# Kernel tuning notes

Hardware: AMD Instinct MI355X
Metric: run time of the kernel (lower is better)

Reference implementation:

```python
import jax, jax.numpy as jnp
import numpy as np

N_NONZERO = 32      # n_nonzero_coefs
TAU = 0.01
LAMBDA_INIT = -5.0  # reg_coeff = softplus(lambda)


def setup_inputs() -> dict:
    key = jax.random.key(0)
    k1, k2 = jax.random.split(key)
    X = jax.random.normal(k1, (64, 1024, 1024), dtype=jnp.float32)
    y = jax.random.normal(k2, (64, 1024, 1), dtype=jnp.float32)
    return {"X": X, "y": y}


def _omp_fit_forward(X, y):
    # Faithful translation of fit() (omp with hard straight-through top-1)
    # followed by forward() reconstruction D @ coef.
    reg = jax.nn.softplus(jnp.asarray(LAMBDA_INIT, jnp.float32)).astype(X.dtype)
    B, L, A = X.shape
    ones = jnp.ones((B, L, 1), X.dtype)
    Dfull = jnp.concatenate([X, ones], axis=-1)   # [B, L, A+1] (bias column)
    D = Dfull[0]                                   # shared dictionary [L, A+1]
    n_atoms = A + 1
    y2 = y[:, :, 0]                                # [B, L]
    y_det = jax.lax.stop_gradient(y2)
    residuals = y_det
    # Cache selected_D columns incrementally: each column j is dict @ ret_j,
    # identical math to the original's full recompute every iteration.
    selD = jnp.zeros((B, L, N_NONZERO), X.dtype)
    idx_all = []
    nzW = None
    for i in range(N_NONZERO):
        proj = residuals @ D                                      # [B, A+1]
        soft = jax.nn.softmax(jnp.abs(proj) / TAU, axis=-1)
        idx = jnp.argmax(jnp.abs(proj), axis=-1)                  # detached indices
        onehot = jax.nn.one_hot(jnp.argmax(soft, axis=-1), n_atoms, dtype=X.dtype)
        ret = onehot - jax.lax.stop_gradient(soft) + soft         # straight-through
        new_col = ret @ D.T                                       # [B, L]
        selD = selD.at[:, :, i].set(new_col)
        Di = selD[:, :, :i + 1]                                   # [B, L, i+1]
        DTy = jnp.einsum('blk,bl->bk', Di, y2)[..., None]         # [B, i+1, 1]
        DTD = jnp.einsum('blk,blj->bkj', Di, Di) + reg * jnp.eye(i + 1, dtype=X.dtype)
        nzW = jnp.linalg.solve(DTD, DTy)                          # [B, i+1, 1]
        residuals = y_det - jnp.einsum('blk,bk->bl', Di, nzW[..., 0])
        idx_all.append(idx)
    indices = jnp.stack(idx_all, axis=1)                          # [B, K] int
    W = jnp.zeros((B, n_atoms), X.dtype).at[jnp.arange(B)[:, None], indices].set(nzW[..., 0])
    # forward(): bmm(dict_with_bias, coef)
    recon = jnp.einsum('bla,ba->bl', Dfull, W)[..., None]         # [B, L, 1]
    return recon


def reference(X, y):
    return _omp_fit_forward(X, y)
```

## Files before the change

kernel.cpp:

```cpp
#include <hip/hip_runtime.h>
#include <math.h>

#define NATOMS   1025
#define GSTRIDE  1040
#define GELEMS   (1025*GSTRIDE)
#define NNZ      32
#define NBATCH   64
#define REGL     0.0067153485f

#define DPPF(x, ctrl) __int_as_float(__builtin_amdgcn_update_dpp(0, __float_as_int(x), (ctrl), 0xF, 0xF, false))

__device__ __forceinline__ float wave_max64(float x) {
    x = fmaxf(x, DPPF(x, 0x111));
    x = fmaxf(x, DPPF(x, 0x112));
    x = fmaxf(x, DPPF(x, 0x114));
    x = fmaxf(x, DPPF(x, 0x118));
    x = fmaxf(x, DPPF(x, 0x142));
    x = fmaxf(x, DPPF(x, 0x143));
    return __int_as_float(__builtin_amdgcn_readlane(__float_as_int(x), 63));
}
__device__ __forceinline__ float wave_sum64(float x) {
    x += DPPF(x, 0x111);
    x += DPPF(x, 0x112);
    x += DPPF(x, 0x114);
    x += DPPF(x, 0x118);
    x += DPPF(x, 0x142);
    x += DPPF(x, 0x143);
    return __int_as_float(__builtin_amdgcn_readlane(__float_as_int(x), 63));
}
__device__ __forceinline__ float readlane_f(float x, int l) {
    return __int_as_float(__builtin_amdgcn_readlane(__float_as_int(x), l));
}

__global__ __launch_bounds__(256)
void gramprojy_kernel(const float* __restrict__ X0, const float* __restrict__ y,
                      float* __restrict__ Gout, float* __restrict__ PY,
                      int kLen, int nsplit) {
    __shared__ float lds[8192];
    const int tid = threadIdx.x;

    if ((int)blockIdx.z < nsplit) {
        const int bx = blockIdx.x, by = blockIdx.y, bz = blockIdx.z;
        if (by < bx) return;
        float* As = lds;
        float* Bs = lds + 4096;
        const int a0 = bx * 128, b0 = by * 128;
        float* __restrict__ Gp = Gout + (size_t)bz * GELEMS;
        const int tx = tid & 15;
        const int ty = tid >> 4;
        const int lr = tid >> 5;
        const int lc = (tid & 31) * 4;
        const bool aIn = (a0 + 128) <= 1024;
        const bool bIn = (b0 + 128) <= 1024;

        float acc[8][8];
#pragma unroll
        for (int m = 0; m < 8; ++m)
#pragma unroll
            for (int n = 0; n < 8; ++n) acc[m][n] = 0.0f;

        const int kBase = bz * kLen;
        for (int kc = 0; kc < kLen; kc += 32) {
#pragma unroll
            for (int rr = 0; rr < 4; ++rr) {
                const int r = lr + rr * 8;
                const int l = kBase + kc + r;
                if (aIn) {
                    *(float4*)&As[r * 128 + lc] = *(const float4*)&X0[(size_t)l * 1024 + a0 + lc];
                } else {
#pragma unroll
                    for (int k = 0; k < 4; ++k) {
                        const int col = a0 + lc + k;
                        As[r * 128 + lc + k] = (col < 1024) ? X0[(size_t)l * 1024 + col]
                                                            : (col == 1024 ? 1.0f : 0.0f);
                    }
                }
                if (bIn) {
                    *(float4*)&Bs[r * 128 + lc] = *(const float4*)&X0[(size_t)l * 1024 + b0 + lc];
                } else {
#pragma unroll
                    for (int k = 0; k < 4; ++k) {
                        const int col = b0 + lc + k;
                        Bs[r * 128 + lc + k] = (col < 1024) ? X0[(size_t)l * 1024 + col]
                                                            : (col == 1024 ? 1.0f : 0.0f);
                    }
                }
            }
            __syncthreads();
#pragma unroll 8
            for (int l = 0; l < 32; ++l) {
                float4 a01 = *(const float4*)&As[l * 128 + ty * 8];
                float4 a23 = *(const float4*)&As[l * 128 + ty * 8 + 4];
                float4 bA  = *(const float4*)&Bs[l * 128 + tx * 4];
                float4 bB  = *(const float4*)&Bs[l * 128 + 64 + tx * 4];
                float am[8] = {a01.x, a01.y, a01.z, a01.w, a23.x, a23.y, a23.z, a23.w};
                float bn[8] = {bA.x, bA.y, bA.z, bA.w, bB.x, bB.y, bB.z, bB.w};
#pragma unroll
                for (int m = 0; m < 8; ++m)
#pragma unroll
                    for (int n = 0; n < 8; ++n)
                        acc[m][n] += am[m] * bn[n];
            }
            __syncthreads();
        }

#pragma unroll
        for (int m = 0; m < 8; ++m) {
            const int a = a0 + ty * 8 + m;
            if (a >= NATOMS) continue;
            const int bAc = b0 + tx * 4;
            const int bBc = b0 + 64 + tx * 4;
            if (bAc < GSTRIDE) {
                *(float4*)&Gp[(size_t)a * GSTRIDE + bAc] =
                    make_float4(acc[m][0], acc[m][1], acc[m][2], acc[m][3]);
            }
            if (bBc < GSTRIDE) {
                *(float4*)&Gp[(size_t)a * GSTRIDE + bBc] =
                    make_float4(acc[m][4], acc[m][5], acc[m][6], acc[m][7]);
            }
        }
        if (bx != by) {
#pragma unroll
            for (int n = 0; n < 8; ++n) {
                const int colg = b0 + ((n < 4) ? (tx * 4 + n) : (64 + tx * 4 + (n - 4)));
                if (colg >= NATOMS) continue;
                const int a = a0 + ty * 8;
                *(float4*)&Gp[(size_t)colg * GSTRIDE + a] =
                    make_float4(acc[0][n], acc[1][n], acc[2][n], acc[3][n]);
                *(float4*)&Gp[(size_t)colg * GSTRIDE + a + 4] =
                    make_float4(acc[4][n], acc[5][n], acc[6][n], acc[7][n]);
            }
        }
    } else {
        const int pw = blockIdx.y * 9 + blockIdx.x;
        if (pw >= 68) return;
        const int a0 = (pw % 17) * 64;
        const int b0 = (pw / 17) * 16;
        float* Ds = lds;
        float* Ys = lds + 2048;
        const int tx = tid & 15;
        const int ty = tid >> 4;
        const bool aIn = (a0 + 64) <= 1024;

        float acc[4] = {0.0f, 0.0f, 0.0f, 0.0f};

        for (int kc = 0; kc < 1024; kc += 32) {
            {
                const int r  = tid >> 4;
                const int c4 = (tid & 15) * 4;
#pragma unroll
                for (int rr = 0; rr < 2; ++rr) {
                    const int row = r + rr * 16;
                    const int l = kc + row;
                    if (aIn) {
                        *(float4*)&Ds[row * 64 + c4] = *(const float4*)&X0[(size_t)l * 1024 + a0 + c4];
                    } else {
#pragma unroll
                        for (int k = 0; k < 4; ++k) {
                            const int col = a0 + c4 + k;
                            Ds[row * 64 + c4 + k] = (col < 1024) ? X0[(size_t)l * 1024 + col]
                                                                 : (col == 1024 ? 1.0f : 0.0f);
                        }
                    }
                }
            }
            for (int e = tid; e < 512; e += 256) {
                const int l = e & 31, bb = e >> 5;
                Ys[l * 17 + bb] = y[(size_t)(b0 + bb) * 1024 + kc + l];
            }
            __syncthreads();
#pragma unroll 8
            for (int l = 0; l < 32; ++l) {
                const float yv = Ys[l * 17 + ty];
                float4 dv = *(const float4*)&Ds[l * 64 + tx * 4];
                acc[0] += yv * dv.x; acc[1] += yv * dv.y;
                acc[2] += yv * dv.z; acc[3] += yv * dv.w;
            }
            __syncthreads();
        }
        const int a = a0 + tx * 4;
        if (a < GSTRIDE) {
            *(float4*)&PY[(size_t)(b0 + ty) * GSTRIDE + a] =
                make_float4(acc[0], acc[1], acc[2], acc[3]);
        }
    }
}

template <int NS>
__global__ __launch_bounds__(512)
void omp_kernel(const float* __restrict__ Gp, const float* __restrict__ PY,
                int* __restrict__ idxOut, float* __restrict__ wOut) {
    __shared__ float rowsLds[NNZ][GSTRIDE];
    __shared__ float pyLds[1040];
    __shared__ float diagLds[1040];
    __shared__ float redV[2][8];
    __shared__ int   redI[2][8];

    const int b = blockIdx.x, tid = threadIdx.x;
    const int lane = tid & 63, wid = tid >> 6;

    float ainv[32];
#pragma unroll
    for (int m = 0; m < 32; ++m) ainv[m] = 0.0f;
    float wvr = 0.0f, rhsr = 0.0f;
    int   myIdx = 0;

    {
        float4 z4 = make_float4(0.f, 0.f, 0.f, 0.f);
        float4* rz = (float4*)rowsLds;
        for (int u = tid; u < NNZ * GSTRIDE / 4; u += 512) rz[u] = z4;
        const float* pyg = PY + (size_t)b * GSTRIDE;
        for (int u = tid; u < 1040; u += 512) pyLds[u] = pyg[u];
        float d0 = 0.f, d1 = 0.f, d2 = 0.f;
#pragma unroll
        for (int z = 0; z < NS; ++z) {
            const float* gz = Gp + (size_t)z * GELEMS;
            d0 += gz[(size_t)tid * (GSTRIDE + 1)];
            d1 += gz[(size_t)(tid + 512) * (GSTRIDE + 1)];
            if (tid == 511) d2 += gz[(size_t)1024 * (GSTRIDE + 1)];
        }
        diagLds[tid] = d0;
        diagLds[tid + 512] = d1;
        if (tid == 511) diagLds[1024] = d2;
    }
    __syncthreads();

    float p0 = pyLds[tid], p1 = pyLds[tid + 512];
    float p2 = (tid == 511) ? pyLds[1024] : 0.0f;

    {
        float best = fabsf(p0); int bidx = tid;
        { float v = fabsf(p1); if (v > best) { best = v; bidx = tid + 512; } }
        if (tid == 511) { float v = fabsf(p2); if (v > best) { best = v; bidx = 1024; } }
        const float wmax = wave_max64(best);
        const unsigned long long mask = __ballot(best == wmax);
        const int fl = __ffsll((unsigned long long)mask) - 1;
        const int widx = __builtin_amdgcn_readlane(bidx, fl);
        if (lane == 0) { redV[0][wid] = wmax; redI[0][wid] = widx; }
    }
    __syncthreads();

    for (int i = 0; i < NNZ; ++i) {
        const int par = i & 1;

        float bv_ = redV[par][0]; int sel = redI[par][0];
#pragma unroll
        for (int q = 1; q < 8; ++q) {
            if (redV[par][q] > bv_ || (redV[par][q] == bv_ && redI[par][q] < sel)) {
                bv_ = redV[par][q]; sel = redI[par][q];
            }
        }
        const float pysel = pyLds[sel];

        float rA0 = 0.f, rA1 = 0.f, rA2 = 0.f, rA3 = 0.f;
        float rB0 = 0.f, rB1 = 0.f, rB2 = 0.f, rB3 = 0.f;
        float rA4 = 0.f, rA5 = 0.f, rA6 = 0.f, rA7 = 0.f;
        float rB4 = 0.f, rB5 = 0.f, rB6 = 0.f, rB7 = 0.f;
        float rC = 0.f;
        if (i < NNZ - 1) {
            const size_t rowoff = (size_t)sel * GSTRIDE;
            const float* g0 = Gp + rowoff;
            rA0 = g0[tid];            rB0 = g0[tid + 512];
            if (NS > 1) { const float* g = g0 + (size_t)1 * GELEMS; rA1 = g[tid]; rB1 = g[tid + 512]; }
            if (NS > 2) { const float* g = g0 + (size_t)2 * GELEMS; rA2 = g[tid]; rB2 = g[tid + 512]; }
            if (NS > 3) { const float* g = g0 + (size_t)3 * GELEMS; rA3 = g[tid]; rB3 = g[tid + 512]; }
            if (NS > 4) { const float* g = g0 + (size_t)4 * GELEMS; rA4 = g[tid]; rB4 = g[tid + 512]; }
            if (NS > 5) { const float* g = g0 + (size_t)5 * GELEMS; rA5 = g[tid]; rB5 = g[tid + 512]; }
            if (NS > 6) { const float* g = g0 + (size_t)6 * GELEMS; rA6 = g[tid]; rB6 = g[tid + 512]; }
            if (NS > 7) { const float* g = g0 + (size_t)7 * GELEMS; rA7 = g[tid]; rB7 = g[tid + 512]; }
            if (tid == 511) {
#pragma unroll
                for (int z = 0; z < NS; ++z) rC += Gp[(size_t)z * GELEMS + rowoff + 1024];
            }
        }

        const float bvl = (lane < 32) ? rowsLds[lane][sel] : 0.0f;
        float u0 = 0.f, u1 = 0.f, u2 = 0.f, u3 = 0.f;
#pragma unroll
        for (int m = 0; m < 32; m += 4) {
            u0 = fmaf(ainv[m + 0], rowsLds[m + 0][sel], u0);
            u1 = fmaf(ainv[m + 1], rowsLds[m + 1][sel], u1);
            u2 = fmaf(ainv[m + 2], rowsLds[m + 2][sel], u2);
            u3 = fmaf(ainv[m + 3], rowsLds[m + 3][sel], u3);
        }
        const float uacc = (u0 + u1) + (u2 + u3);
        const float t = wave_sum64(bvl * uacc);
        const float s = wave_sum64(rhsr * uacc);
        const float dinv = 1.0f / (diagLds[sel] + REGL - t);
        const float beta = dinv * (pysel - s);
        const float uvb = (lane == i) ? -1.0f : uacc;
#pragma unroll
        for (int m = 0; m < 32; ++m)
            ainv[m] = fmaf(uvb * dinv, readlane_f(uvb, m), ainv[m]);
        wvr = (lane == i) ? beta : fmaf(-uacc, beta, wvr);
        rhsr = (lane == i) ? pysel : rhsr;
        if (tid == i) myIdx = sel;

        if (i == NNZ - 1) break;

        float z0 = 0.f, z1 = 0.f, z2 = 0.f;
        for (int jb = 0; jb < NNZ; jb += 8) {
            if (jb >= i) break;
#pragma unroll
            for (int jj = 0; jj < 8; ++jj) {
                const int j = jb + jj;
                const float uj = readlane_f(uvb, j);
                z0 = fmaf(uj, rowsLds[j][tid],       z0);
                z1 = fmaf(uj, rowsLds[j][tid + 512], z1);
                if (tid == 511) z2 = fmaf(uj, rowsLds[j][1024], z2);
            }
        }
        const float r0 = ((rA0 + rA1) + (rA2 + rA3)) + ((rA4 + rA5) + (rA6 + rA7));
        const float r1 = ((rB0 + rB1) + (rB2 + rB3)) + ((rB4 + rB5) + (rB6 + rB7));
        p0 = fmaf(beta, z0, p0); p0 = fmaf(-beta, r0, p0);
        p1 = fmaf(beta, z1, p1); p1 = fmaf(-beta, r1, p1);
        if (tid == 511) { p2 = fmaf(beta, z2, p2); p2 = fmaf(-beta, rC, p2); }

        rowsLds[i][tid]       = r0;
        rowsLds[i][tid + 512] = r1;
        if (tid == 511) rowsLds[i][1024] = rC;

        {
            float best = fabsf(p0); int bidx = tid;
            { float v = fabsf(p1); if (v > best) { best = v; bidx = tid + 512; } }
            if (tid == 511) { float v = fabsf(p2); if (v > best) { best = v; bidx = 1024; } }
            const float wmax = wave_max64(best);
            const unsigned long long mask = __ballot(best == wmax);
            const int fl = __ffsll((unsigned long long)mask) - 1;
            const int widx = __builtin_amdgcn_readlane(bidx, fl);
            if (lane == 0) { redV[par ^ 1][wid] = wmax; redI[par ^ 1][wid] = widx; }
        }
        __syncthreads();
    }

    if (tid < NNZ) {
        idxOut[b * NNZ + tid] = myIdx;
        wOut[b * NNZ + tid] = wvr;
    }
}

__global__ __launch_bounds__(256)
void recon_kernel(const float* __restrict__ X, const int* __restrict__ idxIn,
                  const float* __restrict__ wIn, float* __restrict__ out) {
    __shared__ float Wd[1025];
    __shared__ float wval[NNZ];
    __shared__ int   widx[NNZ];
    __shared__ float biasS;
    const int b = blockIdx.x >> 2, chunk = blockIdx.x & 3;
    const int tid = threadIdx.x;
    for (int u = tid; u < 1025; u += 256) Wd[u] = 0.0f;
    __syncthreads();
    if (tid == 0) {
#pragma unroll
        for (int i = 0; i < NNZ; ++i) Wd[idxIn[b * NNZ + i]] = wIn[b * NNZ + i];
        float bias = 0.0f;
#pragma unroll
        for (int i = 0; i < NNZ; ++i) {
            const int gi = idxIn[b * NNZ + i];
            const float v = Wd[gi];
            Wd[gi] = 0.0f;
            const bool isOnes = (gi == 1024);
            if (isOnes) bias += v;
            widx[i] = isOnes ? 0 : gi;
            wval[i] = isOnes ? 0.0f : v;
        }
        biasS = bias;
    }
    __syncthreads();
    const int l = chunk * 256 + tid;
    const float* __restrict__ xr = X + (size_t)b * 1024 * 1024 + (size_t)l * 1024;
    float a0 = biasS, a1 = 0.f, a2 = 0.f, a3 = 0.f;
#pragma unroll
    for (int i = 0; i < NNZ; i += 4) {
        a0 = fmaf(xr[widx[i + 0]], wval[i + 0], a0);
        a1 = fmaf(xr[widx[i + 1]], wval[i + 1], a1);
        a2 = fmaf(xr[widx[i + 2]], wval[i + 2], a2);
        a3 = fmaf(xr[widx[i + 3]], wval[i + 3], a3);
    }
    out[(size_t)b * 1024 + l] = (a0 + a1) + (a2 + a3);
}

extern "C" void kernel_launch(void* const* d_in, const int* in_sizes, int n_in,
                              void* d_out, int out_size, void* d_ws, size_t ws_size,
                              hipStream_t stream) {
    const float* X = (const float*)d_in[0];
    const float* y = (const float*)d_in[1];
    float* out = (float*)d_out;
    float* ws = (float*)d_ws;

    const size_t fixed = (size_t)64 * GSTRIDE + NBATCH * NNZ * 2 + 64;
    const size_t need8 = ((size_t)GELEMS * 8 + fixed) * sizeof(float);
    const size_t need4 = ((size_t)GELEMS * 4 + fixed) * sizeof(float);
    const int nsplit = (ws_size >= need8) ? 8 : ((ws_size >= need4) ? 4 : 1);
    const int kLen = 1024 / nsplit;

    float* Gp = ws;
    float* PY = ws + (size_t)GELEMS * nsplit;
    float* wOut = PY + (size_t)64 * GSTRIDE;
    int* idxOut = (int*)(wOut + NBATCH * NNZ);

    gramprojy_kernel<<<dim3(9, 9, nsplit + 1), 256, 0, stream>>>(X, y, Gp, PY, kLen, nsplit);
    if (nsplit == 8)      omp_kernel<8><<<NBATCH, 512, 0, stream>>>(Gp, PY, idxOut, wOut);
    else if (nsplit == 4) omp_kernel<4><<<NBATCH, 512, 0, stream>>>(Gp, PY, idxOut, wOut);
    else                  omp_kernel<1><<<NBATCH, 512, 0, stream>>>(Gp, PY, idxOut, wOut);
    recon_kernel<<<NBATCH * 4, 256, 0, stream>>>(X, idxOut, wOut, out);
}
```

Before: 221.2 us.

## Keep selected Gram rows in registers and fully unroll OMP iterations

Each thread now holds the 32 selected Gram-row entries for its two columns in register arrays instead of a 32x1040 LDS table, and the iteration loop is fully unrolled by macro so those arrays can be indexed statically. The selected column's entries are broadcast through a small shared vector, which adds an extra barrier per iteration. The maximum Gram split drops from 8 to 4, so the partial-Gram reduction per row load does less work but the Gram build runs with fewer splits. Register pressure rises sharply (64 extra floats per thread at 512 threads), which risks spills.

```diff
diff --git a/kernel.cpp b/kernel.cpp
--- a/kernel.cpp
+++ b/kernel.cpp
@@ -190,27 +190,28 @@
 __global__ __launch_bounds__(512)
 void omp_kernel(const float* __restrict__ Gp, const float* __restrict__ PY,
                 int* __restrict__ idxOut, float* __restrict__ wOut) {
-    __shared__ float rowsLds[NNZ][GSTRIDE];
     __shared__ float pyLds[1040];
     __shared__ float diagLds[1040];
+    __shared__ float bvec[32];
+    __shared__ float row1024[NNZ];
     __shared__ float redV[2][8];
     __shared__ int   redI[2][8];
 
     const int b = blockIdx.x, tid = threadIdx.x;
     const int lane = tid & 63, wid = tid >> 6;
 
+    float rr0[NNZ], rr1[NNZ];
     float ainv[32];
 #pragma unroll
-    for (int m = 0; m < 32; ++m) ainv[m] = 0.0f;
-    float wvr = 0.0f, rhsr = 0.0f;
+    for (int m = 0; m < 32; ++m) { ainv[m] = 0.f; rr0[m] = 0.f; rr1[m] = 0.f; }
+    float wvr = 0.f, rhsr = 0.f;
     int   myIdx = 0;
 
     {
-        float4 z4 = make_float4(0.f, 0.f, 0.f, 0.f);
-        float4* rz = (float4*)rowsLds;
-        for (int u = tid; u < NNZ * GSTRIDE / 4; u += 512) rz[u] = z4;
         const float* pyg = PY + (size_t)b * GSTRIDE;
-        for (int u = tid; u < 1040; u += 512) pyLds[u] = pyg[u];
+        pyLds[tid] = pyg[tid];
+        pyLds[tid + 512] = pyg[tid + 512];
+        if (tid < 16) pyLds[1024 + tid] = pyg[1024 + tid];
         float d0 = 0.f, d1 = 0.f, d2 = 0.f;
 #pragma unroll
         for (int z = 0; z < NS; ++z) {
@@ -222,11 +223,12 @@
         diagLds[tid] = d0;
         diagLds[tid + 512] = d1;
         if (tid == 511) diagLds[1024] = d2;
+        if (tid < 32) { bvec[tid] = 0.f; row1024[tid] = 0.f; }
     }
     __syncthreads();
 
     float p0 = pyLds[tid], p1 = pyLds[tid + 512];
-    float p2 = (tid == 511) ? pyLds[1024] : 0.0f;
+    float p2 = (tid == 511) ? pyLds[1024] : 0.f;
 
     {
         float best = fabsf(p0); int bidx = tid;
@@ -240,98 +242,108 @@
     }
     __syncthreads();
 
-    for (int i = 0; i < NNZ; ++i) {
-        const int par = i & 1;
-
-        float bv_ = redV[par][0]; int sel = redI[par][0];
-#pragma unroll
-        for (int q = 1; q < 8; ++q) {
-            if (redV[par][q] > bv_ || (redV[par][q] == bv_ && redI[par][q] < sel)) {
-                bv_ = redV[par][q]; sel = redI[par][q];
-            }
-        }
-        const float pysel = pyLds[sel];
-
-        float rA0 = 0.f, rA1 = 0.f, rA2 = 0.f, rA3 = 0.f;
-        float rB0 = 0.f, rB1 = 0.f, rB2 = 0.f, rB3 = 0.f;
-        float rA4 = 0.f, rA5 = 0.f, rA6 = 0.f, rA7 = 0.f;
-        float rB4 = 0.f, rB5 = 0.f, rB6 = 0.f, rB7 = 0.f;
-        float rC = 0.f;
-        if (i < NNZ - 1) {
-            const size_t rowoff = (size_t)sel * GSTRIDE;
-            const float* g0 = Gp + rowoff;
-            rA0 = g0[tid];            rB0 = g0[tid + 512];
-            if (NS > 1) { const float* g = g0 + (size_t)1 * GELEMS; rA1 = g[tid]; rB1 = g[tid + 512]; }
-            if (NS > 2) { const float* g = g0 + (size_t)2 * GELEMS; rA2 = g[tid]; rB2 = g[tid + 512]; }
-            if (NS > 3) { const float* g = g0 + (size_t)3 * GELEMS; rA3 = g[tid]; rB3 = g[tid + 512]; }
-            if (NS > 4) { const float* g = g0 + (size_t)4 * GELEMS; rA4 = g[tid]; rB4 = g[tid + 512]; }
-            if (NS > 5) { const float* g = g0 + (size_t)5 * GELEMS; rA5 = g[tid]; rB5 = g[tid + 512]; }
-            if (NS > 6) { const float* g = g0 + (size_t)6 * GELEMS; rA6 = g[tid]; rB6 = g[tid + 512]; }
-            if (NS > 7) { const float* g = g0 + (size_t)7 * GELEMS; rA7 = g[tid]; rB7 = g[tid + 512]; }
-            if (tid == 511) {
-#pragma unroll
-                for (int z = 0; z < NS; ++z) rC += Gp[(size_t)z * GELEMS + rowoff + 1024];
-            }
-        }
-
-        const float bvl = (lane < 32) ? rowsLds[lane][sel] : 0.0f;
-        float u0 = 0.f, u1 = 0.f, u2 = 0.f, u3 = 0.f;
-#pragma unroll
-        for (int m = 0; m < 32; m += 4) {
-            u0 = fmaf(ainv[m + 0], rowsLds[m + 0][sel], u0);
-            u1 = fmaf(ainv[m + 1], rowsLds[m + 1][sel], u1);
-            u2 = fmaf(ainv[m + 2], rowsLds[m + 2][sel], u2);
-            u3 = fmaf(ainv[m + 3], rowsLds[m + 3][sel], u3);
-        }
-        const float uacc = (u0 + u1) + (u2 + u3);
-        const float t = wave_sum64(bvl * uacc);
-        const float s = wave_sum64(rhsr * uacc);
-        const float dinv = 1.0f / (diagLds[sel] + REGL - t);
-        const float beta = dinv * (pysel - s);
-        const float uvb = (lane == i) ? -1.0f : uacc;
-#pragma unroll
-        for (int m = 0; m < 32; ++m)
-            ainv[m] = fmaf(uvb * dinv, readlane_f(uvb, m), ainv[m]);
-        wvr = (lane == i) ? beta : fmaf(-uacc, beta, wvr);
-        rhsr = (lane == i) ? pysel : rhsr;
-        if (tid == i) myIdx = sel;
-
-        if (i == NNZ - 1) break;
-
-        float z0 = 0.f, z1 = 0.f, z2 = 0.f;
-        for (int jb = 0; jb < NNZ; jb += 8) {
-            if (jb >= i) break;
-#pragma unroll
-            for (int jj = 0; jj < 8; ++jj) {
-                const int j = jb + jj;
-                const float uj = readlane_f(uvb, j);
-                z0 = fmaf(uj, rowsLds[j][tid],       z0);
-                z1 = fmaf(uj, rowsLds[j][tid + 512], z1);
-                if (tid == 511) z2 = fmaf(uj, rowsLds[j][1024], z2);
-            }
-        }
-        const float r0 = ((rA0 + rA1) + (rA2 + rA3)) + ((rA4 + rA5) + (rA6 + rA7));
-        const float r1 = ((rB0 + rB1) + (rB2 + rB3)) + ((rB4 + rB5) + (rB6 + rB7));
-        p0 = fmaf(beta, z0, p0); p0 = fmaf(-beta, r0, p0);
-        p1 = fmaf(beta, z1, p1); p1 = fmaf(-beta, r1, p1);
-        if (tid == 511) { p2 = fmaf(beta, z2, p2); p2 = fmaf(-beta, rC, p2); }
-
-        rowsLds[i][tid]       = r0;
-        rowsLds[i][tid + 512] = r1;
-        if (tid == 511) rowsLds[i][1024] = rC;
-
-        {
-            float best = fabsf(p0); int bidx = tid;
-            { float v = fabsf(p1); if (v > best) { best = v; bidx = tid + 512; } }
-            if (tid == 511) { float v = fabsf(p2); if (v > best) { best = v; bidx = 1024; } }
-            const float wmax = wave_max64(best);
-            const unsigned long long mask = __ballot(best == wmax);
-            const int fl = __ffsll((unsigned long long)mask) - 1;
-            const int widx = __builtin_amdgcn_readlane(bidx, fl);
-            if (lane == 0) { redV[par ^ 1][wid] = wmax; redI[par ^ 1][wid] = widx; }
-        }
-        __syncthreads();
-    }
+#define OMP_ITER(I)                                                            \
+    {                                                                          \
+        const int par = (I) & 1;                                               \
+        float bv_ = redV[par][0]; int sel = redI[par][0];                      \
+        _Pragma("unroll")                                                      \
+        for (int q = 1; q < 8; ++q) {                                          \
+            if (redV[par][q] > bv_ ||                                          \
+                (redV[par][q] == bv_ && redI[par][q] < sel)) {                 \
+                bv_ = redV[par][q]; sel = redI[par][q];                        \
+            }                                                                  \
+        }                                                                      \
+        const float pysel = pyLds[sel];                                        \
+        float rA0=0.f,rA1=0.f,rA2=0.f,rA3=0.f;                                 \
+        float rB0=0.f,rB1=0.f,rB2=0.f,rB3=0.f,rC=0.f;                          \
+        if ((I) < NNZ - 1) {                                                   \
+            const size_t ro = (size_t)sel * GSTRIDE;                           \
+            { const float* g = Gp + ro; rA0 = g[tid]; rB0 = g[tid + 512]; }    \
+            if (NS > 1) { const float* g = Gp + ro + (size_t)1 * GELEMS;       \
+                          rA1 = g[tid]; rB1 = g[tid + 512]; }                  \
+            if (NS > 2) { const float* g = Gp + ro + (size_t)2 * GELEMS;       \
+                          rA2 = g[tid]; rB2 = g[tid + 512]; }                  \
+            if (NS > 3) { const float* g = Gp + ro + (size_t)3 * GELEMS;       \
+                          rA3 = g[tid]; rB3 = g[tid + 512]; }                  \
+            if (tid == 511) {                                                  \
+                _Pragma("unroll")                                              \
+                for (int z = 0; z < NS; ++z)                                   \
+                    rC += Gp[(size_t)z * GELEMS + ro + 1024];                  \
+            }                                                                  \
+        }                                                                      \
+        if (sel == 1024) {                                                     \
+            if (tid < 32) bvec[tid] = row1024[tid];                            \
+        } else if (tid == (sel & 511)) {                                       \
+            if (sel >> 9) {                                                    \
+                _Pragma("unroll")                                              \
+                for (int m = 0; m < 32; ++m) bvec[m] = rr1[m];                 \
+            } else {                                                           \
+                _Pragma("unroll")                                              \
+                for (int m = 0; m < 32; ++m) bvec[m] = rr0[m];                 \
+            }                                                                  \
+        }                                                                      \
+        __syncthreads();                               \
+        const float bvl = (lane < 32) ? bvec[lane] : 0.f;                      \
+        float u0 = 0.f, u1 = 0.f;                                              \
+        _Pragma("unroll")                                                      \
+        for (int m = 0; m < 32; m += 2) {                                      \
+            u0 = fmaf(ainv[m],     bvec[m],     u0);                           \
+            u1 = fmaf(ainv[m + 1], bvec[m + 1], u1);                           \
+        }                                                                      \
+        const float uacc = u0 + u1;                                            \
+        const float t = wave_sum64(bvl * uacc);                                \
+        const float s = wave_sum64(rhsr * uacc);                               \
+        const float dinv = 1.0f / (diagLds[sel] + REGL - t);                   \
+        const float beta = dinv * (pysel - s);                                 \
+        const float uvb = (lane == (I)) ? -1.0f : uacc;                        \
+        _Pragma("unroll")                                                      \
+        for (int m = 0; m < 32; ++m)                                           \
+            ainv[m] = fmaf(uvb * dinv, readlane_f(uvb, m), ainv[m]);           \
+        wvr  = (lane == (I)) ? beta  : fmaf(-uacc, beta, wvr);                 \
+        rhsr = (lane == (I)) ? pysel : rhsr;                                   \
+        if (tid == (I)) myIdx = sel;                                           \
+        if ((I) < NNZ - 1) {                                                   \
+            float z0 = 0.f, z1 = 0.f, z2 = 0.f;                                \
+            _Pragma("unroll")                                                  \
+            for (int j = 0; j < NNZ - 1; ++j) {                                \
+                if (j < (I)) {                                                 \
+                    const float uj = readlane_f(uvb, j);                       \
+                    z0 = fmaf(uj, rr0[j], z0);                                 \
+                    z1 = fmaf(uj, rr1[j], z1);                                 \
+                    if (tid == 511) z2 = fmaf(uj, row1024[j], z2);             \
+                }                                                              \
+            }                                                                  \
+            const float r0 = (rA0 + rA1) + (rA2 + rA3);                        \
+            const float r1 = (rB0 + rB1) + (rB2 + rB3);                        \
+            p0 = fmaf(beta, z0, p0); p0 = fmaf(-beta, r0, p0);                 \
+            p1 = fmaf(beta, z1, p1); p1 = fmaf(-beta, r1, p1);                 \
+            if (tid == 511) { p2 = fmaf(beta, z2, p2);                         \
+                              p2 = fmaf(-beta, rC, p2); }                      \
+            rr0[(I)] = r0; rr1[(I)] = r1;                                      \
+            if (tid == 511) row1024[(I)] = rC;                                 \
+            float best = fabsf(p0); int bidx = tid;                            \
+            { float v = fabsf(p1); if (v > best) { best = v; bidx = tid + 512; } } \
+            if (tid == 511) { float v = fabsf(p2);                             \
+                              if (v > best) { best = v; bidx = 1024; } }       \
+            const float wmax = wave_max64(best);                               \
+            const unsigned long long mask = __ballot(best == wmax);            \
+            const int fl = __ffsll((unsigned long long)mask) - 1;              \
+            const int widx = __builtin_amdgcn_readlane(bidx, fl);              \
+            if (lane == 0) { redV[par ^ 1][wid] = wmax;                        \
+                             redI[par ^ 1][wid] = widx; }                      \
+            __syncthreads();                    \
+        }                                                                      \
+    }
+
+    OMP_ITER(0)  OMP_ITER(1)  OMP_ITER(2)  OMP_ITER(3)
+    OMP_ITER(4)  OMP_ITER(5)  OMP_ITER(6)  OMP_ITER(7)
+    OMP_ITER(8)  OMP_ITER(9)  OMP_ITER(10) OMP_ITER(11)
+    OMP_ITER(12) OMP_ITER(13) OMP_ITER(14) OMP_ITER(15)
+    OMP_ITER(16) OMP_ITER(17) OMP_ITER(18) OMP_ITER(19)
+    OMP_ITER(20) OMP_ITER(21) OMP_ITER(22) OMP_ITER(23)
+    OMP_ITER(24) OMP_ITER(25) OMP_ITER(26) OMP_ITER(27)
+    OMP_ITER(28) OMP_ITER(29) OMP_ITER(30) OMP_ITER(31)
+#undef OMP_ITER
 
     if (tid < NNZ) {
         idxOut[b * NNZ + tid] = myIdx;
@@ -389,9 +401,8 @@
     float* ws = (float*)d_ws;
 
     const size_t fixed = (size_t)64 * GSTRIDE + NBATCH * NNZ * 2 + 64;
-    const size_t need8 = ((size_t)GELEMS * 8 + fixed) * sizeof(float);
     const size_t need4 = ((size_t)GELEMS * 4 + fixed) * sizeof(float);
-    const int nsplit = (ws_size >= need8) ? 8 : ((ws_size >= need4) ? 4 : 1);
+    const int nsplit = (ws_size >= need4) ? 4 : 1;
     const int kLen = 1024 / nsplit;
 
     float* Gp = ws;
@@ -400,8 +411,7 @@
     int* idxOut = (int*)(wOut + NBATCH * NNZ);
 
     gramprojy_kernel<<<dim3(9, 9, nsplit + 1), 256, 0, stream>>>(X, y, Gp, PY, kLen, nsplit);
-    if (nsplit == 8)      omp_kernel<8><<<NBATCH, 512, 0, stream>>>(Gp, PY, idxOut, wOut);
-    else if (nsplit == 4) omp_kernel<4><<<NBATCH, 512, 0, stream>>>(Gp, PY, idxOut, wOut);
-    else                  omp_kernel<1><<<NBATCH, 512, 0, stream>>>(Gp, PY, idxOut, wOut);
+    if (nsplit == 4) omp_kernel<4><<<NBATCH, 512, 0, stream>>>(Gp, PY, idxOut, wOut);
+    else             omp_kernel<1><<<NBATCH, 512, 0, stream>>>(Gp, PY, idxOut, wOut);
     recon_kernel<<<NBATCH * 4, 256, 0, stream>>>(X, idxOut, wOut, out);
 }
```

After: 179.8 us. 18.7% less time.

## Run OMP loop with one wavefront per batch and drop cross-wave reductions

Applied to the files above, without the earlier changes.

The OMP kernel now runs each batch on a single 64-lane wavefront instead of 512 threads. Each lane holds 16 projection values in registers and does the argmax fully inside the wave with DPP, so the LDS cross-wave reduction is gone. Rows of Ainv are gathered with readlane instead of LDS reads, and the Gram split count drops from 8 to at most 4, which lowers gram partial-sum traffic. The cost is far less parallelism per batch: 64 waves in total do the serial per-atom work, and the Gram row loads and the z accumulation are each spread over only 64 lanes.

```diff
diff --git a/kernel.cpp b/kernel.cpp
--- a/kernel.cpp
+++ b/kernel.cpp
@@ -4,21 +4,13 @@
 #define NATOMS   1025
 #define GSTRIDE  1040
 #define GELEMS   (1025*GSTRIDE)
+#define RSTRIDE  1026
 #define NNZ      32
 #define NBATCH   64
 #define REGL     0.0067153485f
 
 #define DPPF(x, ctrl) __int_as_float(__builtin_amdgcn_update_dpp(0, __float_as_int(x), (ctrl), 0xF, 0xF, false))
 
-__device__ __forceinline__ float wave_max64(float x) {
-    x = fmaxf(x, DPPF(x, 0x111));
-    x = fmaxf(x, DPPF(x, 0x112));
-    x = fmaxf(x, DPPF(x, 0x114));
-    x = fmaxf(x, DPPF(x, 0x118));
-    x = fmaxf(x, DPPF(x, 0x142));
-    x = fmaxf(x, DPPF(x, 0x143));
-    return __int_as_float(__builtin_amdgcn_readlane(__float_as_int(x), 63));
-}
 __device__ __forceinline__ float wave_sum64(float x) {
     x += DPPF(x, 0x111);
     x += DPPF(x, 0x112);
@@ -30,6 +22,17 @@
 }
 __device__ __forceinline__ float readlane_f(float x, int l) {
     return __int_as_float(__builtin_amdgcn_readlane(__float_as_int(x), l));
+}
+__device__ __forceinline__ void wave_argmax64(float& v, int& idx) {
+#define AM_STEP(ctrl) {                                                        \
+        float ov = DPPF(v, ctrl);                                              \
+        int   oi = __builtin_amdgcn_update_dpp(0, idx, (ctrl), 0xF, 0xF, false);\
+        if (ov > v || (ov == v && oi < idx)) { v = ov; idx = oi; } }
+    AM_STEP(0x111) AM_STEP(0x112) AM_STEP(0x114) AM_STEP(0x118)
+    AM_STEP(0x142) AM_STEP(0x143)
+#undef AM_STEP
+    v   = readlane_f(v, 63);
+    idx = __builtin_amdgcn_readlane(idx, 63);
 }
 
 __global__ __launch_bounds__(256)
@@ -187,103 +190,87 @@
 }
 
 template <int NS>
-__global__ __launch_bounds__(512)
+__global__ __launch_bounds__(64)
 void omp_kernel(const float* __restrict__ Gp, const float* __restrict__ PY,
                 int* __restrict__ idxOut, float* __restrict__ wOut) {
-    __shared__ float rowsLds[NNZ][GSTRIDE];
-    __shared__ float pyLds[1040];
-    __shared__ float diagLds[1040];
-    __shared__ float redV[2][8];
-    __shared__ int   redI[2][8];
-
-    const int b = blockIdx.x, tid = threadIdx.x;
-    const int lane = tid & 63, wid = tid >> 6;
+    __shared__ float rowsLds[NNZ][RSTRIDE];
+    __shared__ float pyLds[NATOMS];
+    __shared__ float diagLds[NATOMS];
+
+    const int b = blockIdx.x;
+    const int lane = threadIdx.x;
 
     float ainv[32];
 #pragma unroll
-    for (int m = 0; m < 32; ++m) ainv[m] = 0.0f;
-    float wvr = 0.0f, rhsr = 0.0f;
+    for (int m = 0; m < 32; ++m) ainv[m] = 0.f;
+    float wvr = 0.f, rhsr = 0.f;
     int   myIdx = 0;
 
     {
-        float4 z4 = make_float4(0.f, 0.f, 0.f, 0.f);
-        float4* rz = (float4*)rowsLds;
-        for (int u = tid; u < NNZ * GSTRIDE / 4; u += 512) rz[u] = z4;
+        float4* rz = (float4*)&rowsLds[0][0];
+        for (int u = lane; u < NNZ * RSTRIDE / 4; u += 64)
+            rz[u] = make_float4(0.f, 0.f, 0.f, 0.f);
         const float* pyg = PY + (size_t)b * GSTRIDE;
-        for (int u = tid; u < 1040; u += 512) pyLds[u] = pyg[u];
-        float d0 = 0.f, d1 = 0.f, d2 = 0.f;
-#pragma unroll
-        for (int z = 0; z < NS; ++z) {
-            const float* gz = Gp + (size_t)z * GELEMS;
-            d0 += gz[(size_t)tid * (GSTRIDE + 1)];
-            d1 += gz[(size_t)(tid + 512) * (GSTRIDE + 1)];
-            if (tid == 511) d2 += gz[(size_t)1024 * (GSTRIDE + 1)];
-        }
-        diagLds[tid] = d0;
-        diagLds[tid + 512] = d1;
-        if (tid == 511) diagLds[1024] = d2;
+        for (int u = lane; u < NATOMS; u += 64) {
+            pyLds[u] = pyg[u];
+            float d = 0.f;
+#pragma unroll
+            for (int z = 0; z < NS; ++z)
+                d += Gp[(size_t)z * GELEMS + (size_t)u * (GSTRIDE + 1)];
+            diagLds[u] = d;
+        }
     }
     __syncthreads();
 
-    float p0 = pyLds[tid], p1 = pyLds[tid + 512];
-    float p2 = (tid == 511) ? pyLds[1024] : 0.0f;
-
+    float2 pr[8];
+#pragma unroll
+    for (int k = 0; k < 8; ++k)
+        pr[k] = *(const float2*)&pyLds[2 * lane + 128 * k];
+    float p1024 = (lane == 0) ? pyLds[1024] : 0.f;
+
+    float bv; int sel;
     {
-        float best = fabsf(p0); int bidx = tid;
-        { float v = fabsf(p1); if (v > best) { best = v; bidx = tid + 512; } }
-        if (tid == 511) { float v = fabsf(p2); if (v > best) { best = v; bidx = 1024; } }
-        const float wmax = wave_max64(best);
-        const unsigned long long mask = __ballot(best == wmax);
-        const int fl = __ffsll((unsigned long long)mask) - 1;
-        const int widx = __builtin_amdgcn_readlane(bidx, fl);
-        if (lane == 0) { redV[0][wid] = wmax; redI[0][wid] = widx; }
-    }
-    __syncthreads();
+        bv = fabsf(pr[0].x); sel = 2 * lane;
+        { float v = fabsf(pr[0].y); if (v > bv) { bv = v; sel = 2 * lane + 1; } }
+#pragma unroll
+        for (int k = 1; k < 8; ++k) {
+            float vx = fabsf(pr[k].x);
+            if (vx > bv) { bv = vx; sel = 2 * lane + 128 * k; }
+            float vy = fabsf(pr[k].y);
+            if (vy > bv) { bv = vy; sel = 2 * lane + 128 * k + 1; }
+        }
+        if (lane == 0) { float v = fabsf(p1024); if (v > bv) { bv = v; sel = 1024; } }
+        wave_argmax64(bv, sel);
+    }
 
     for (int i = 0; i < NNZ; ++i) {
-        const int par = i & 1;
-
-        float bv_ = redV[par][0]; int sel = redI[par][0];
-#pragma unroll
-        for (int q = 1; q < 8; ++q) {
-            if (redV[par][q] > bv_ || (redV[par][q] == bv_ && redI[par][q] < sel)) {
-                bv_ = redV[par][q]; sel = redI[par][q];
-            }
-        }
         const float pysel = pyLds[sel];
 
-        float rA0 = 0.f, rA1 = 0.f, rA2 = 0.f, rA3 = 0.f;
-        float rB0 = 0.f, rB1 = 0.f, rB2 = 0.f, rB3 = 0.f;
-        float rA4 = 0.f, rA5 = 0.f, rA6 = 0.f, rA7 = 0.f;
-        float rB4 = 0.f, rB5 = 0.f, rB6 = 0.f, rB7 = 0.f;
-        float rC = 0.f;
+        float2 sv[8]; float s1024 = 0.f;
+#pragma unroll
+        for (int k = 0; k < 8; ++k) sv[k] = make_float2(0.f, 0.f);
         if (i < NNZ - 1) {
-            const size_t rowoff = (size_t)sel * GSTRIDE;
-            const float* g0 = Gp + rowoff;
-            rA0 = g0[tid];            rB0 = g0[tid + 512];
-            if (NS > 1) { const float* g = g0 + (size_t)1 * GELEMS; rA1 = g[tid]; rB1 = g[tid + 512]; }
-            if (NS > 2) { const float* g = g0 + (size_t)2 * GELEMS; rA2 = g[tid]; rB2 = g[tid + 512]; }
-            if (NS > 3) { const float* g = g0 + (size_t)3 * GELEMS; rA3 = g[tid]; rB3 = g[tid + 512]; }
-            if (NS > 4) { const float* g = g0 + (size_t)4 * GELEMS; rA4 = g[tid]; rB4 = g[tid + 512]; }
-            if (NS > 5) { const float* g = g0 + (size_t)5 * GELEMS; rA5 = g[tid]; rB5 = g[tid + 512]; }
-            if (NS > 6) { const float* g = g0 + (size_t)6 * GELEMS; rA6 = g[tid]; rB6 = g[tid + 512]; }
-            if (NS > 7) { const float* g = g0 + (size_t)7 * GELEMS; rA7 = g[tid]; rB7 = g[tid + 512]; }
-            if (tid == 511) {
-#pragma unroll
-                for (int z = 0; z < NS; ++z) rC += Gp[(size_t)z * GELEMS + rowoff + 1024];
-            }
-        }
-
-        const float bvl = (lane < 32) ? rowsLds[lane][sel] : 0.0f;
-        float u0 = 0.f, u1 = 0.f, u2 = 0.f, u3 = 0.f;
-#pragma unroll
-        for (int m = 0; m < 32; m += 4) {
-            u0 = fmaf(ainv[m + 0], rowsLds[m + 0][sel], u0);
-            u1 = fmaf(ainv[m + 1], rowsLds[m + 1][sel], u1);
-            u2 = fmaf(ainv[m + 2], rowsLds[m + 2][sel], u2);
-            u3 = fmaf(ainv[m + 3], rowsLds[m + 3][sel], u3);
-        }
-        const float uacc = (u0 + u1) + (u2 + u3);
+            const size_t ro = (size_t)sel * GSTRIDE;
+#pragma unroll
+            for (int z = 0; z < NS; ++z) {
+                const float* g = Gp + (size_t)z * GELEMS + ro;
+#pragma unroll
+                for (int k = 0; k < 8; ++k) {
+                    const float2 t2 = *(const float2*)(g + 2 * lane + 128 * k);
+                    sv[k].x += t2.x; sv[k].y += t2.y;
+                }
+                if (lane == 0) s1024 += g[1024];
+            }
+        }
+
+        const float bvl = (lane < 32) ? rowsLds[lane][sel] : 0.f;
+        float u0 = 0.f, u1 = 0.f;
+#pragma unroll
+        for (int m = 0; m < 32; m += 2) {
+            u0 = fmaf(ainv[m],     readlane_f(bvl, m),     u0);
+            u1 = fmaf(ainv[m + 1], readlane_f(bvl, m + 1), u1);
+        }
+        const float uacc = u0 + u1;
         const float t = wave_sum64(bvl * uacc);
         const float s = wave_sum64(rhsr * uacc);
         const float dinv = 1.0f / (diagLds[sel] + REGL - t);
@@ -292,50 +279,54 @@
 #pragma unroll
         for (int m = 0; m < 32; ++m)
             ainv[m] = fmaf(uvb * dinv, readlane_f(uvb, m), ainv[m]);
-        wvr = (lane == i) ? beta : fmaf(-uacc, beta, wvr);
+        wvr  = (lane == i) ? beta  : fmaf(-uacc, beta, wvr);
         rhsr = (lane == i) ? pysel : rhsr;
-        if (tid == i) myIdx = sel;
+        if (lane == i) myIdx = sel;
 
         if (i == NNZ - 1) break;
 
-        float z0 = 0.f, z1 = 0.f, z2 = 0.f;
-        for (int jb = 0; jb < NNZ; jb += 8) {
-            if (jb >= i) break;
-#pragma unroll
-            for (int jj = 0; jj < 8; ++jj) {
-                const int j = jb + jj;
-                const float uj = readlane_f(uvb, j);
-                z0 = fmaf(uj, rowsLds[j][tid],       z0);
-                z1 = fmaf(uj, rowsLds[j][tid + 512], z1);
-                if (tid == 511) z2 = fmaf(uj, rowsLds[j][1024], z2);
-            }
-        }
-        const float r0 = ((rA0 + rA1) + (rA2 + rA3)) + ((rA4 + rA5) + (rA6 + rA7));
-        const float r1 = ((rB0 + rB1) + (rB2 + rB3)) + ((rB4 + rB5) + (rB6 + rB7));
-        p0 = fmaf(beta, z0, p0); p0 = fmaf(-beta, r0, p0);
-        p1 = fmaf(beta, z1, p1); p1 = fmaf(-beta, r1, p1);
-        if (tid == 511) { p2 = fmaf(beta, z2, p2); p2 = fmaf(-beta, rC, p2); }
-
-        rowsLds[i][tid]       = r0;
-        rowsLds[i][tid + 512] = r1;
-        if (tid == 511) rowsLds[i][1024] = rC;
-
-        {
-            float best = fabsf(p0); int bidx = tid;
-            { float v = fabsf(p1); if (v > best) { best = v; bidx = tid + 512; } }
-            if (tid == 511) { float v = fabsf(p2); if (v > best) { best = v; bidx = 1024; } }
-            const float wmax = wave_max64(best);
-            const unsigned long long mask = __ballot(best == wmax);
-            const int fl = __ffsll((unsigned long long)mask) - 1;
-            const int widx = __builtin_amdgcn_readlane(bidx, fl);
-            if (lane == 0) { redV[par ^ 1][wid] = wmax; redI[par ^ 1][wid] = widx; }
-        }
+        float2 zz[8]; float z1024 = 0.f;
+#pragma unroll
+        for (int k = 0; k < 8; ++k) zz[k] = make_float2(0.f, 0.f);
+        for (int j = 0; j < i; ++j) {
+            const float uj = readlane_f(uvb, j);
+#pragma unroll
+            for (int k = 0; k < 8; ++k) {
+                const float2 g = *(const float2*)&rowsLds[j][2 * lane + 128 * k];
+                zz[k].x = fmaf(uj, g.x, zz[k].x);
+                zz[k].y = fmaf(uj, g.y, zz[k].y);
+            }
+            if (lane == 0) z1024 = fmaf(uj, rowsLds[j][1024], z1024);
+        }
+#pragma unroll
+        for (int k = 0; k < 8; ++k) {
+            pr[k].x = fmaf(beta, zz[k].x, pr[k].x); pr[k].x = fmaf(-beta, sv[k].x, pr[k].x);
+            pr[k].y = fmaf(beta, zz[k].y, pr[k].y); pr[k].y = fmaf(-beta, sv[k].y, pr[k].y);
+        }
+        if (lane == 0) { p1024 = fmaf(beta, z1024, p1024); p1024 = fmaf(-beta, s1024, p1024); }
+
+#pragma unroll
+        for (int k = 0; k < 8; ++k)
+            *(float2*)&rowsLds[i][2 * lane + 128 * k] = sv[k];
+        if (lane == 0) rowsLds[i][1024] = s1024;
         __syncthreads();
-    }
-
-    if (tid < NNZ) {
-        idxOut[b * NNZ + tid] = myIdx;
-        wOut[b * NNZ + tid] = wvr;
+
+        bv = fabsf(pr[0].x); sel = 2 * lane;
+        { float v = fabsf(pr[0].y); if (v > bv) { bv = v; sel = 2 * lane + 1; } }
+#pragma unroll
+        for (int k = 1; k < 8; ++k) {
+            float vx = fabsf(pr[k].x);
+            if (vx > bv) { bv = vx; sel = 2 * lane + 128 * k; }
+            float vy = fabsf(pr[k].y);
+            if (vy > bv) { bv = vy; sel = 2 * lane + 128 * k + 1; }
+        }
+        if (lane == 0) { float v = fabsf(p1024); if (v > bv) { bv = v; sel = 1024; } }
+        wave_argmax64(bv, sel);
+    }
+
+    if (lane < NNZ) {
+        idxOut[b * NNZ + lane] = myIdx;
+        wOut[b * NNZ + lane] = wvr;
     }
 }
 
@@ -389,9 +380,8 @@
     float* ws = (float*)d_ws;
 
     const size_t fixed = (size_t)64 * GSTRIDE + NBATCH * NNZ * 2 + 64;
-    const size_t need8 = ((size_t)GELEMS * 8 + fixed) * sizeof(float);
     const size_t need4 = ((size_t)GELEMS * 4 + fixed) * sizeof(float);
-    const int nsplit = (ws_size >= need8) ? 8 : ((ws_size >= need4) ? 4 : 1);
+    const int nsplit = (ws_size >= need4) ? 4 : 1;
     const int kLen = 1024 / nsplit;
 
     float* Gp = ws;
@@ -400,8 +390,7 @@
     int* idxOut = (int*)(wOut + NBATCH * NNZ);
 
     gramprojy_kernel<<<dim3(9, 9, nsplit + 1), 256, 0, stream>>>(X, y, Gp, PY, kLen, nsplit);
-    if (nsplit == 8)      omp_kernel<8><<<NBATCH, 512, 0, stream>>>(Gp, PY, idxOut, wOut);
-    else if (nsplit == 4) omp_kernel<4><<<NBATCH, 512, 0, stream>>>(Gp, PY, idxOut, wOut);
-    else                  omp_kernel<1><<<NBATCH, 512, 0, stream>>>(Gp, PY, idxOut, wOut);
+    if (nsplit == 4) omp_kernel<4><<<NBATCH, 64, 0, stream>>>(Gp, PY, idxOut, wOut);
+    else             omp_kernel<1><<<NBATCH, 64, 0, stream>>>(Gp, PY, idxOut, wOut);
     recon_kernel<<<NBATCH * 4, 256, 0, stream>>>(X, idxOut, wOut, out);
 }
```

Result: slower. 226.6 us (+2.5%).

## Transpose OMP column cache in LDS and cap Gram split at four

Applied to the files above, without the earlier changes.

Stores the cached Gram rows in LDS transposed (atom-major with stride 33), so gathering the selected atom's column and each thread's own history becomes a contiguous, bank-conflict-free read. The z accumulation loop now runs exactly i iterations instead of blocks of eight. The per-wave argmax becomes a fused value/index DPP reduction that drops the ballot step. The Gram split is capped at four partial slices, which halves the global row loads per OMP iteration but makes each partial GEMM in the first kernel longer.

```diff
diff --git a/kernel.cpp b/kernel.cpp
--- a/kernel.cpp
+++ b/kernel.cpp
@@ -4,21 +4,13 @@
 #define NATOMS   1025
 #define GSTRIDE  1040
 #define GELEMS   (1025*GSTRIDE)
+#define CSTRIDE  33
 #define NNZ      32
 #define NBATCH   64
 #define REGL     0.0067153485f
 
 #define DPPF(x, ctrl) __int_as_float(__builtin_amdgcn_update_dpp(0, __float_as_int(x), (ctrl), 0xF, 0xF, false))
 
-__device__ __forceinline__ float wave_max64(float x) {
-    x = fmaxf(x, DPPF(x, 0x111));
-    x = fmaxf(x, DPPF(x, 0x112));
-    x = fmaxf(x, DPPF(x, 0x114));
-    x = fmaxf(x, DPPF(x, 0x118));
-    x = fmaxf(x, DPPF(x, 0x142));
-    x = fmaxf(x, DPPF(x, 0x143));
-    return __int_as_float(__builtin_amdgcn_readlane(__float_as_int(x), 63));
-}
 __device__ __forceinline__ float wave_sum64(float x) {
     x += DPPF(x, 0x111);
     x += DPPF(x, 0x112);
@@ -190,7 +182,7 @@
 __global__ __launch_bounds__(512)
 void omp_kernel(const float* __restrict__ Gp, const float* __restrict__ PY,
                 int* __restrict__ idxOut, float* __restrict__ wOut) {
-    __shared__ float rowsLds[NNZ][GSTRIDE];
+    __shared__ float colT[NATOMS * CSTRIDE];
     __shared__ float pyLds[1040];
     __shared__ float diagLds[1040];
     __shared__ float redV[2][8];
@@ -201,16 +193,16 @@
 
     float ainv[32];
 #pragma unroll
-    for (int m = 0; m < 32; ++m) ainv[m] = 0.0f;
-    float wvr = 0.0f, rhsr = 0.0f;
+    for (int m = 0; m < 32; ++m) ainv[m] = 0.f;
+    float wvr = 0.f, rhsr = 0.f;
     int   myIdx = 0;
 
     {
-        float4 z4 = make_float4(0.f, 0.f, 0.f, 0.f);
-        float4* rz = (float4*)rowsLds;
-        for (int u = tid; u < NNZ * GSTRIDE / 4; u += 512) rz[u] = z4;
+        for (int u = tid; u < NATOMS * CSTRIDE; u += 512) colT[u] = 0.f;
         const float* pyg = PY + (size_t)b * GSTRIDE;
-        for (int u = tid; u < 1040; u += 512) pyLds[u] = pyg[u];
+        pyLds[tid] = pyg[tid];
+        pyLds[tid + 512] = pyg[tid + 512];
+        if (tid < 16) pyLds[1024 + tid] = pyg[1024 + tid];
         float d0 = 0.f, d1 = 0.f, d2 = 0.f;
 #pragma unroll
         for (int z = 0; z < NS; ++z) {
@@ -226,17 +218,22 @@
     __syncthreads();
 
     float p0 = pyLds[tid], p1 = pyLds[tid + 512];
-    float p2 = (tid == 511) ? pyLds[1024] : 0.0f;
+    float p2 = (tid == 511) ? pyLds[1024] : 0.f;
 
     {
         float best = fabsf(p0); int bidx = tid;
         { float v = fabsf(p1); if (v > best) { best = v; bidx = tid + 512; } }
         if (tid == 511) { float v = fabsf(p2); if (v > best) { best = v; bidx = 1024; } }
-        const float wmax = wave_max64(best);
-        const unsigned long long mask = __ballot(best == wmax);
-        const int fl = __ffsll((unsigned long long)mask) - 1;
-        const int widx = __builtin_amdgcn_readlane(bidx, fl);
-        if (lane == 0) { redV[0][wid] = wmax; redI[0][wid] = widx; }
+        float wv_ = best; int wi_ = bidx;
+#define AM_STEP(ctrl) {                                                        \
+        float ov = DPPF(wv_, ctrl);                                            \
+        int   oi = __builtin_amdgcn_update_dpp(0, wi_, (ctrl), 0xF, 0xF, false);\
+        if (ov > wv_ || (ov == wv_ && oi < wi_)) { wv_ = ov; wi_ = oi; } }
+        AM_STEP(0x111) AM_STEP(0x112) AM_STEP(0x114) AM_STEP(0x118)
+        AM_STEP(0x142) AM_STEP(0x143)
+        wv_ = readlane_f(wv_, 63);
+        wi_ = __builtin_amdgcn_readlane(wi_, 63);
+        if (lane == 0) { redV[0][wid] = wv_; redI[0][wid] = wi_; }
     }
     __syncthreads();
 
@@ -253,37 +250,28 @@
         const float pysel = pyLds[sel];
 
         float rA0 = 0.f, rA1 = 0.f, rA2 = 0.f, rA3 = 0.f;
-        float rB0 = 0.f, rB1 = 0.f, rB2 = 0.f, rB3 = 0.f;
-        float rA4 = 0.f, rA5 = 0.f, rA6 = 0.f, rA7 = 0.f;
-        float rB4 = 0.f, rB5 = 0.f, rB6 = 0.f, rB7 = 0.f;
-        float rC = 0.f;
+        float rB0 = 0.f, rB1 = 0.f, rB2 = 0.f, rB3 = 0.f, rC = 0.f;
         if (i < NNZ - 1) {
-            const size_t rowoff = (size_t)sel * GSTRIDE;
-            const float* g0 = Gp + rowoff;
-            rA0 = g0[tid];            rB0 = g0[tid + 512];
-            if (NS > 1) { const float* g = g0 + (size_t)1 * GELEMS; rA1 = g[tid]; rB1 = g[tid + 512]; }
-            if (NS > 2) { const float* g = g0 + (size_t)2 * GELEMS; rA2 = g[tid]; rB2 = g[tid + 512]; }
-            if (NS > 3) { const float* g = g0 + (size_t)3 * GELEMS; rA3 = g[tid]; rB3 = g[tid + 512]; }
-            if (NS > 4) { const float* g = g0 + (size_t)4 * GELEMS; rA4 = g[tid]; rB4 = g[tid + 512]; }
-            if (NS > 5) { const float* g = g0 + (size_t)5 * GELEMS; rA5 = g[tid]; rB5 = g[tid + 512]; }
-            if (NS > 6) { const float* g = g0 + (size_t)6 * GELEMS; rA6 = g[tid]; rB6 = g[tid + 512]; }
-            if (NS > 7) { const float* g = g0 + (size_t)7 * GELEMS; rA7 = g[tid]; rB7 = g[tid + 512]; }
+            const size_t ro = (size_t)sel * GSTRIDE;
+            { const float* g = Gp + ro;                      rA0 = g[tid]; rB0 = g[tid + 512]; }
+            if (NS > 1) { const float* g = Gp + ro + (size_t)1 * GELEMS; rA1 = g[tid]; rB1 = g[tid + 512]; }
+            if (NS > 2) { const float* g = Gp + ro + (size_t)2 * GELEMS; rA2 = g[tid]; rB2 = g[tid + 512]; }
+            if (NS > 3) { const float* g = Gp + ro + (size_t)3 * GELEMS; rA3 = g[tid]; rB3 = g[tid + 512]; }
             if (tid == 511) {
 #pragma unroll
-                for (int z = 0; z < NS; ++z) rC += Gp[(size_t)z * GELEMS + rowoff + 1024];
-            }
-        }
-
-        const float bvl = (lane < 32) ? rowsLds[lane][sel] : 0.0f;
-        float u0 = 0.f, u1 = 0.f, u2 = 0.f, u3 = 0.f;
-#pragma unroll
-        for (int m = 0; m < 32; m += 4) {
-            u0 = fmaf(ainv[m + 0], rowsLds[m + 0][sel], u0);
-            u1 = fmaf(ainv[m + 1], rowsLds[m + 1][sel], u1);
-            u2 = fmaf(ainv[m + 2], rowsLds[m + 2][sel], u2);
-            u3 = fmaf(ainv[m + 3], rowsLds[m + 3][sel], u3);
-        }
-        const float uacc = (u0 + u1) + (u2 + u3);
+                for (int z = 0; z < NS; ++z) rC += Gp[(size_t)z * GELEMS + ro + 1024];
+            }
+        }
+
+        const float* csel = &colT[sel * CSTRIDE];
+        const float bvl = (lane < 32) ? csel[lane] : 0.f;
+        float u0 = 0.f, u1 = 0.f;
+#pragma unroll
+        for (int m = 0; m < 32; m += 2) {
+            u0 = fmaf(ainv[m],     csel[m],     u0);
+            u1 = fmaf(ainv[m + 1], csel[m + 1], u1);
+        }
+        const float uacc = u0 + u1;
         const float t = wave_sum64(bvl * uacc);
         const float s = wave_sum64(rhsr * uacc);
         const float dinv = 1.0f / (diagLds[sel] + REGL - t);
@@ -292,46 +280,45 @@
 #pragma unroll
         for (int m = 0; m < 32; ++m)
             ainv[m] = fmaf(uvb * dinv, readlane_f(uvb, m), ainv[m]);
-        wvr = (lane == i) ? beta : fmaf(-uacc, beta, wvr);
+        wvr  = (lane == i) ? beta  : fmaf(-uacc, beta, wvr);
         rhsr = (lane == i) ? pysel : rhsr;
         if (tid == i) myIdx = sel;
 
         if (i == NNZ - 1) break;
 
         float z0 = 0.f, z1 = 0.f, z2 = 0.f;
-        for (int jb = 0; jb < NNZ; jb += 8) {
-            if (jb >= i) break;
-#pragma unroll
-            for (int jj = 0; jj < 8; ++jj) {
-                const int j = jb + jj;
-                const float uj = readlane_f(uvb, j);
-                z0 = fmaf(uj, rowsLds[j][tid],       z0);
-                z1 = fmaf(uj, rowsLds[j][tid + 512], z1);
-                if (tid == 511) z2 = fmaf(uj, rowsLds[j][1024], z2);
-            }
-        }
-        const float r0 = ((rA0 + rA1) + (rA2 + rA3)) + ((rA4 + rA5) + (rA6 + rA7));
-        const float r1 = ((rB0 + rB1) + (rB2 + rB3)) + ((rB4 + rB5) + (rB6 + rB7));
+        const float* c0 = &colT[tid * CSTRIDE];
+        const float* c1 = &colT[(tid + 512) * CSTRIDE];
+        for (int j = 0; j < i; ++j) {
+            const float uj = readlane_f(uvb, j);
+            z0 = fmaf(uj, c0[j], z0);
+            z1 = fmaf(uj, c1[j], z1);
+            if (tid == 511) z2 = fmaf(uj, colT[1024 * CSTRIDE + j], z2);
+        }
+        const float r0 = (rA0 + rA1) + (rA2 + rA3);
+        const float r1 = (rB0 + rB1) + (rB2 + rB3);
         p0 = fmaf(beta, z0, p0); p0 = fmaf(-beta, r0, p0);
         p1 = fmaf(beta, z1, p1); p1 = fmaf(-beta, r1, p1);
         if (tid == 511) { p2 = fmaf(beta, z2, p2); p2 = fmaf(-beta, rC, p2); }
 
-        rowsLds[i][tid]       = r0;
-        rowsLds[i][tid + 512] = r1;
-        if (tid == 511) rowsLds[i][1024] = rC;
+        colT[tid * CSTRIDE + i] = r0;
+        colT[(tid + 512) * CSTRIDE + i] = r1;
+        if (tid == 511) colT[1024 * CSTRIDE + i] = rC;
 
         {
             float best = fabsf(p0); int bidx = tid;
             { float v = fabsf(p1); if (v > best) { best = v; bidx = tid + 512; } }
             if (tid == 511) { float v = fabsf(p2); if (v > best) { best = v; bidx = 1024; } }
-            const float wmax = wave_max64(best);
-            const unsigned long long mask = __ballot(best == wmax);
-            const int fl = __ffsll((unsigned long long)mask) - 1;
-            const int widx = __builtin_amdgcn_readlane(bidx, fl);
-            if (lane == 0) { redV[par ^ 1][wid] = wmax; redI[par ^ 1][wid] = widx; }
+            float wv_ = best; int wi_ = bidx;
+            AM_STEP(0x111) AM_STEP(0x112) AM_STEP(0x114) AM_STEP(0x118)
+            AM_STEP(0x142) AM_STEP(0x143)
+            wv_ = readlane_f(wv_, 63);
+            wi_ = __builtin_amdgcn_readlane(wi_, 63);
+            if (lane == 0) { redV[par ^ 1][wid] = wv_; redI[par ^ 1][wid] = wi_; }
         }
         __syncthreads();
     }
+#undef AM_STEP
 
     if (tid < NNZ) {
         idxOut[b * NNZ + tid] = myIdx;
@@ -389,9 +376,8 @@
     float* ws = (float*)d_ws;
 
     const size_t fixed = (size_t)64 * GSTRIDE + NBATCH * NNZ * 2 + 64;
-    const size_t need8 = ((size_t)GELEMS * 8 + fixed) * sizeof(float);
     const size_t need4 = ((size_t)GELEMS * 4 + fixed) * sizeof(float);
-    const int nsplit = (ws_size >= need8) ? 8 : ((ws_size >= need4) ? 4 : 1);
+    const int nsplit = (ws_size >= need4) ? 4 : 1;
     const int kLen = 1024 / nsplit;
 
     float* Gp = ws;
@@ -400,8 +386,7 @@
     int* idxOut = (int*)(wOut + NBATCH * NNZ);
 
     gramprojy_kernel<<<dim3(9, 9, nsplit + 1), 256, 0, stream>>>(X, y, Gp, PY, kLen, nsplit);
-    if (nsplit == 8)      omp_kernel<8><<<NBATCH, 512, 0, stream>>>(Gp, PY, idxOut, wOut);
-    else if (nsplit == 4) omp_kernel<4><<<NBATCH, 512, 0, stream>>>(Gp, PY, idxOut, wOut);
-    else                  omp_kernel<1><<<NBATCH, 512, 0, stream>>>(Gp, PY, idxOut, wOut);
+    if (nsplit == 4) omp_kernel<4><<<NBATCH, 512, 0, stream>>>(Gp, PY, idxOut, wOut);
+    else             omp_kernel<1><<<NBATCH, 512, 0, stream>>>(Gp, PY, idxOut, wOut);
     recon_kernel<<<NBATCH * 4, 256, 0, stream>>>(X, idxOut, wOut, out);
 }
```

After: 214.2 us. -3.2%, faster.
